# Performance work log

Hardware: AMD Instinct MI355X
Metric: run time of the kernel (lower is better)

The kernel has to match this reference:

```python
import jax, jax.numpy as jnp
import numpy as np

N, E = 10000, 160000
HID, EDIM = 256, 128
EPS = 1e-5


def _layernorm(x, g, b):
    mu = jnp.mean(x, axis=-1, keepdims=True)
    var = jnp.mean(jnp.square(x - mu), axis=-1, keepdims=True)
    return (x - mu) * jax.lax.rsqrt(var + EPS) * g + b


def setup_inputs() -> dict:
    key = jax.random.key(0)
    ks = jax.random.split(key, 12)
    cat_dim = 2 * HID + EDIM  # 640

    def lin(k, fan_in, fan_out):
        kw, kb = jax.random.split(k)
        lim = 1.0 / np.sqrt(fan_in)
        W = jax.random.uniform(kw, (fan_in, fan_out), jnp.float32, -lim, lim)
        b = jax.random.uniform(kb, (fan_out,), jnp.float32, -lim, lim)
        return W, b

    We1, be1 = lin(ks[0], cat_dim, EDIM)
    We2, be2 = lin(ks[1], EDIM, EDIM)
    Wv1, bv1 = lin(ks[2], cat_dim, HID)
    Wv2, bv2 = lin(ks[3], HID, HID)

    return {
        "h": jax.random.normal(ks[4], (N, HID), jnp.float32),
        "e": jax.random.normal(ks[5], (E, EDIM), jnp.float32),
        "edge_index": jax.random.randint(ks[6], (2, E), 0, N, jnp.int64),
        "We1": We1, "be1": be1, "We2": We2, "be2": be2,
        "Wv1": Wv1, "bv1": bv1, "Wv2": Wv2, "bv2": bv2,
        "ne_g": jnp.ones((EDIM,), jnp.float32), "ne_b": jnp.zeros((EDIM,), jnp.float32),
        "nv_g": jnp.ones((HID,), jnp.float32), "nv_b": jnp.zeros((HID,), jnp.float32),
    }


def reference(h, e, edge_index, We1, be1, We2, be2, Wv1, bv1, Wv2, bv2,
              ne_g, ne_b, nv_g, nv_b):
    # Eval mode: dropout and edge_drop are identity.
    src, dst = edge_index[0], edge_index[1]
    h_src = h[src]  # [E, HID] gather
    h_dst = h[dst]  # [E, HID] gather

    # Edge update: phi_e(concat) -> residual + LayerNorm
    xe = jnp.concatenate([h_src, h_dst, e], axis=-1)  # [E, 2H+ED]
    e_msg = jax.nn.gelu(xe @ We1 + be1, approximate=False) @ We2 + be2
    e_new = _layernorm(e + e_msg, ne_g, ne_b)

    # Node update: phi_v(concat with updated e) -> scatter_mean -> residual + LN
    xv = jnp.concatenate([h_src, h_dst, e_new], axis=-1)
    m = jax.nn.gelu(xv @ Wv1 + bv1, approximate=False) @ Wv2 + bv2  # [E, HID]
    agg = jax.ops.segment_sum(m, dst, num_segments=h.shape[0])
    counts = jax.ops.segment_sum(jnp.ones((m.shape[0], 1), m.dtype), dst,
                                 num_segments=h.shape[0])
    agg = agg / jnp.maximum(counts, 1.0)
    h_new = _layernorm(h + agg, nv_g, nv_b)
    return (h_new, e_new)
```

## Files before the change

kernel.cpp:

```cpp
#include <hip/hip_runtime.h>
#include <hip/hip_bf16.h>

#define NNODE 10000
#define NEDGE 160000
#define HIDD  256
#define ED    128
#define CAT   640

typedef short bf8 __attribute__((ext_vector_type(8)));
typedef short bf4 __attribute__((ext_vector_type(4)));
typedef float f4  __attribute__((ext_vector_type(4)));
typedef unsigned int u32;

__device__ __forceinline__ float bf2f(ushort u) {
    return __uint_as_float(((unsigned)u) << 16);
}
__device__ __forceinline__ ushort f2bf(float f) {
    unsigned u = __float_as_uint(f);
    return (ushort)((u + 0x7fffu + ((u >> 16) & 1u)) >> 16);
}
__device__ __forceinline__ float gelu_fast(float x) {
    float x2 = x * x;
    float u = 0.7978845608028654f * x * (1.0f + 0.044715f * x2);
    float au = fabsf(u);
    float ex = __expf(2.0f * au);
    float t = 1.0f - 2.0f / (1.0f + ex);
    t = copysignf(t, u);
    return 0.5f * x * (1.0f + t);
}
__device__ __forceinline__ int clampi(int v) {
    return ((unsigned)v >= (unsigned)NNODE) ? 0 : v;
}
__device__ __forceinline__ int getidx(const int* ei, bool i64, int pos) {
    int v = i64 ? ei[2 * pos] : ei[pos];
    return clampi(v);
}
__device__ __forceinline__ float loadf(const void* p, size_t idx, bool f32) {
    return f32 ? ((const float*)p)[idx] : bf2f(((const ushort*)p)[idx]);
}
__device__ __forceinline__ bf8 load8(const void* p, size_t idx, bool f32) {
    if (f32) {
        const float* fp = (const float*)p + idx;
        f4 lo = *(const f4*)fp, hi = *(const f4*)(fp + 4);
        bf8 r;
        r[0] = (short)f2bf(lo[0]); r[1] = (short)f2bf(lo[1]);
        r[2] = (short)f2bf(lo[2]); r[3] = (short)f2bf(lo[3]);
        r[4] = (short)f2bf(hi[0]); r[5] = (short)f2bf(hi[1]);
        r[6] = (short)f2bf(hi[2]); r[7] = (short)f2bf(hi[3]);
        return r;
    }
    return *(const bf8*)((const ushort*)p + idx);
}
__device__ __forceinline__ void storef(void* p, size_t idx, float v, bool f32) {
    if (f32) ((float*)p)[idx] = v;
    else     ((ushort*)p)[idx] = f2bf(v);
}
__device__ __forceinline__ void fadd_native(float* p, float v) {
    unsafeAtomicAdd(p, v);
}
__device__ __forceinline__ void detect_local(const u32* h_u32, const u32* ei_u32,
                                             u32* sf) {
    if (threadIdx.x < 64) {
        int t = threadIdx.x;
        u32 e8 = (h_u32[t] >> 7) & 0xFFu;
        bool inw = (e8 >= 100u && e8 <= 150u);
        unsigned long long m = __ballot(inw);
        bool hi_nz = (t < 16) ? (ei_u32[2 * t + 1] != 0u) : false;
        unsigned long long m2 = __ballot(hi_nz);
        if (t == 0) {
            sf[0] = (__popcll(m) < 40) ? 1u : 0u;
            sf[1] = (m2 == 0ull) ? 1u : 0u;
        }
    }
    __syncthreads();
}

#define PREP_B 1280
#define HCONV_B 1250
#define COUNT_B 625
__global__ __launch_bounds__(256) void combo_kernel(
    const void* __restrict__ h, const int* __restrict__ ei,
    const void* __restrict__ We1, const void* __restrict__ We2,
    const void* __restrict__ Wv1, const void* __restrict__ Wv2,
    ushort* __restrict__ WT, ushort* __restrict__ hb,
    u32* __restrict__ cnt, u32* __restrict__ flags)
{
    __shared__ u32 sf[2];
    detect_local((const u32*)h, (const u32*)ei, sf);
    const bool f32 = sf[0] != 0, i64 = sf[1] != 0;
    int b = blockIdx.x, tid = threadIdx.x;

    if (b == 0 && tid == 0) { flags[0] = sf[0]; flags[1] = sf[1]; }

    if (b < PREP_B) {
        int idx = b * 256 + tid;
        if (idx >= 327680) return;
        const void* W; int base, k0, K, Wld;
        if      (idx <  32768) { W = We1; base = 0;      k0 = 0;   K = 256; Wld = 128; }
        else if (idx <  65536) { W = We1; base = 32768;  k0 = 256; K = 256; Wld = 128; }
        else if (idx <  81920) { W = We1; base = 65536;  k0 = 512; K = 128; Wld = 128; }
        else if (idx <  98304) { W = We2; base = 81920;  k0 = 0;   K = 128; Wld = 128; }
        else if (idx < 163840) { W = Wv1; base = 98304;  k0 = 0;   K = 256; Wld = 256; }
        else if (idx < 229376) { W = Wv1; base = 163840; k0 = 256; K = 256; Wld = 256; }
        else if (idx < 262144) { W = Wv1; base = 229376; k0 = 512; K = 128; Wld = 256; }
        else                   { W = Wv2; base = 262144; k0 = 0;   K = 256; Wld = 256; }
        int local = idx - base;
        int k = local & (K - 1);
        int n = local / K;
        WT[idx] = f2bf(loadf(W, (size_t)(k0 + k) * Wld + n, f32));
    } else if (b < PREP_B + HCONV_B) {
        int i = (b - PREP_B) * 256 + tid;
        if (i < NNODE * HIDD / 8)
            *(bf8*)&hb[(size_t)i * 8] = load8(h, (size_t)i * 8, f32);
    } else {
        int i = (b - PREP_B - HCONV_B) * 256 + tid;
        if (i < NEDGE) atomicAdd(&cnt[getidx(ei, i64, NEDGE + i)], 1u);
    }
}

__global__ void scan_kernel(const u32* __restrict__ cnt, int* __restrict__ head) {
    __shared__ u32 part[256];
    __shared__ u32 base[256];
    int t = threadIdx.x;
    u32 s = 0;
    for (int j = 0; j < 40; ++j) {
        int i = t * 40 + j;
        if (i < NNODE) s += cnt[i];
    }
    part[t] = s;
    __syncthreads();
    if (t == 0) {
        u32 run = 0;
        for (int i = 0; i < 256; ++i) { base[i] = run; run += part[i]; }
    }
    __syncthreads();
    u32 run = base[t];
    for (int j = 0; j < 40; ++j) {
        int i = t * 40 + j;
        if (i < NNODE) { head[i] = (int)run; run += cnt[i]; }
    }
}

template<int NB>
__device__ __forceinline__ void qp_body(const ushort* __restrict__ hb,
                                        const ushort* __restrict__ WT,
                                        const void* __restrict__ bias,
                                        ushort* __restrict__ O, int bid, bool f32) {
    const int tid = threadIdx.x;
    const int wid = tid >> 6, lane = tid & 63;
    const int l16 = lane & 15, lg = lane >> 4;
    const int node0 = bid * 64;
    const int N = NB * 64;
    const int n0 = wid * (NB * 16);

    size_t ra[4];
    #pragma unroll
    for (int ai = 0; ai < 4; ++ai) {
        int row = node0 + ai * 16 + l16;
        ra[ai] = (size_t)(row < NNODE ? row : NNODE - 1) * HIDD;
    }
    int bb[NB];
    #pragma unroll
    for (int bi = 0; bi < NB; ++bi) bb[bi] = (n0 + bi * 16 + l16) * HIDD;

    f4 acc[4][NB] = {};
    for (int kc = 0; kc < 4; ++kc) {
        #pragma unroll
        for (int ks = 0; ks < 2; ++ks) {
            int kk = kc * 64 + ks * 32 + lg * 8;
            bf8 b[NB];
            #pragma unroll
            for (int bi = 0; bi < NB; ++bi) b[bi] = *(const bf8*)&WT[bb[bi] + kk];
            #pragma unroll
            for (int ai = 0; ai < 4; ++ai) {
                bf8 a = *(const bf8*)&hb[ra[ai] + kk];
                #pragma unroll
                for (int bi = 0; bi < NB; ++bi)
                    acc[ai][bi] = __builtin_amdgcn_mfma_f32_16x16x32_bf16(a, b[bi], acc[ai][bi], 0, 0, 0);
            }
        }
    }
    #pragma unroll
    for (int bi = 0; bi < NB; ++bi) {
        int col = n0 + bi * 16 + l16;
        int pcol; float badd;
        if constexpr (NB == 4) {
            int hh = col >> 7, c = col & 127;
            badd = (hh == 0) ? loadf(bias, c, f32) : 0.f;
            pcol = hh * 128 + (c & 15) * 8 + (c >> 4);
        } else {
            int hh = col >> 8, c = col & 255;
            badd = (hh == 0) ? loadf(bias, c, f32) : 0.f;
            int nh2 = c >> 7, rem = c & 127, w = rem >> 5, b2 = (rem >> 4) & 1, l = c & 15;
            pcol = hh * 256 + w * 64 + l * 4 + nh2 * 2 + b2;
        }
        #pragma unroll
        for (int ai = 0; ai < 4; ++ai)
            #pragma unroll
            for (int r = 0; r < 4; ++r) {
                int gr = node0 + ai * 16 + lg * 4 + r;
                if (gr < NNODE) O[(size_t)gr * N + pcol] = f2bf(acc[ai][bi][r] + badd);
            }
    }
}

#define QPB ((NNODE + 63) / 64)
#define FILL_B 625
__global__ __launch_bounds__(256) void fillqp_kernel(
    const int* __restrict__ ei, int* __restrict__ head,
    int* __restrict__ perm, int* __restrict__ dsts,
    const ushort* __restrict__ hb, const ushort* __restrict__ WTe,
    const ushort* __restrict__ WTv, const void* __restrict__ be1,
    const void* __restrict__ bv1, ushort* __restrict__ Qab,
    ushort* __restrict__ Pab, const u32* __restrict__ flags)
{
    const bool f32 = flags[0] != 0, i64 = flags[1] != 0;
    int b = blockIdx.x;
    if (b < FILL_B) {
        int i = b * 256 + threadIdx.x;
        if (i < NEDGE) {
            int d = getidx(ei, i64, NEDGE + i);
            int pos = atomicAdd(&head[d], 1);
            perm[pos] = i;
            dsts[pos] = d;
        }
    } else if (b < FILL_B + QPB) {
        qp_body<4>(hb, WTe, be1, Qab, b - FILL_B, f32);
    } else {
        qp_body<8>(hb, WTv, bv1, Pab, b - FILL_B - QPB, f32);
    }
}

#define FWG (NEDGE / 64)
__global__ __launch_bounds__(256) void fused_kernel(
    const void* __restrict__ e, const int* __restrict__ ei,
    const int* __restrict__ perm, const int* __restrict__ dsts,
    const ushort* __restrict__ WT1c,
    const ushort* __restrict__ WT2, const void* __restrict__ be2,
    const ushort* __restrict__ Qab,
    const void* __restrict__ neg, const void* __restrict__ neb,
    const ushort* __restrict__ WvcT,
    const ushort* __restrict__ Pab,
    float* __restrict__ S, void* __restrict__ out,
    const u32* __restrict__ flags)
{
    const bool f32 = flags[0] != 0, i64 = flags[1] != 0;
    __shared__ ushort Asm[64 * 136];
    __shared__ ushort Bsm[128 * 136];
    __shared__ ushort Tsm[64 * 136];
    __shared__ int PermS[64], SrcS[64], DstS[64];

    int orig = blockIdx.x;
    int xcd = orig & 7, slot = orig >> 3;
    int bid = (xcd < 4 ? xcd * 313 : 4 * 313 + (xcd - 4) * 312) + slot;

    const int tid = threadIdx.x;
    const int wid = tid >> 6, lane = tid & 63;
    const int l16 = lane & 15, lg = lane >> 4;
    const int edge0 = bid * 64;
    const int rm = wid * 16;

    if (tid < 64) {
        int eid = perm[edge0 + tid];
        PermS[tid] = eid;
        SrcS[tid] = getidx(ei, i64, eid);
        DstS[tid] = dsts[edge0 + tid];
    }
    __syncthreads();

    #pragma unroll
    for (int j = 0; j < 4; ++j) {
        int s2 = tid + j * 256;
        int r = s2 >> 4, c8 = (s2 & 15) * 8;
        *(bf8*)&Asm[r * 136 + c8] = load8(e, (size_t)PermS[r] * ED + c8, f32);
    }
    #pragma unroll
    for (int it = 0; it < 8; ++it) {
        int s2 = tid + it * 256;
        int n = s2 >> 4, c8 = (s2 & 15) * 8;
        *(bf8*)&Bsm[n * 136 + c8] = *(const bf8*)&WT1c[n * 128 + c8];
    }
    __syncthreads();

    f4 acc[8] = {};
    #pragma unroll
    for (int kc = 0; kc < 2; ++kc)
        #pragma unroll
        for (int ks = 0; ks < 2; ++ks) {
            int ko = kc * 64 + ks * 32 + lg * 8;
            bf8 a = *(const bf8*)&Asm[(rm + l16) * 136 + ko];
            #pragma unroll
            for (int f = 0; f < 8; ++f) {
                bf8 b = *(const bf8*)&Bsm[(f * 16 + l16) * 136 + ko];
                acc[f] = __builtin_amdgcn_mfma_f32_16x16x32_bf16(a, b, acc[f], 0, 0, 0);
            }
        }

    {
        bf8 qs[4], qd[4];
        #pragma unroll
        for (int r = 0; r < 4; ++r) {
            int row = rm + lg * 4 + r;
            qs[r] = *(const bf8*)&Qab[(size_t)SrcS[row] * 256 + l16 * 8];
            qd[r] = *(const bf8*)&Qab[(size_t)DstS[row] * 256 + 128 + l16 * 8];
        }
        #pragma unroll
        for (int f = 0; f < 8; ++f)
            #pragma unroll
            for (int r = 0; r < 4; ++r) {
                float val = acc[f][r] + bf2f((ushort)qs[r][f]) + bf2f((ushort)qd[r][f]);
                Tsm[(rm + lg * 4 + r) * 136 + f * 16 + l16] = f2bf(gelu_fast(val));
            }
    }
    __syncthreads();

    #pragma unroll
    for (int it = 0; it < 8; ++it) {
        int s2 = tid + it * 256;
        int n = s2 >> 4, c8 = (s2 & 15) * 8;
        *(bf8*)&Bsm[n * 136 + c8] = *(const bf8*)&WT2[n * 128 + c8];
    }
    __syncthreads();

    f4 acc2[8] = {};
    #pragma unroll
    for (int kc = 0; kc < 2; ++kc)
        #pragma unroll
        for (int ks = 0; ks < 2; ++ks) {
            int ko = kc * 64 + ks * 32 + lg * 8;
            bf8 a = *(const bf8*)&Tsm[(rm + l16) * 136 + ko];
            #pragma unroll
            for (int f = 0; f < 8; ++f) {
                bf8 b = *(const bf8*)&Bsm[(f * 16 + l16) * 136 + ko];
                acc2[f] = __builtin_amdgcn_mfma_f32_16x16x32_bf16(a, b, acc2[f], 0, 0, 0);
            }
        }

    {
        float v[8][4];
        #pragma unroll
        for (int f = 0; f < 8; ++f) {
            int col = f * 16 + l16;
            float bias = loadf(be2, col, f32);
            #pragma unroll
            for (int r = 0; r < 4; ++r) {
                int row = rm + lg * 4 + r;
                v[f][r] = acc2[f][r] + bias + bf2f(Asm[row * 136 + col]);
            }
        }
        #pragma unroll
        for (int r = 0; r < 4; ++r) {
            float s = 0.f;
            #pragma unroll
            for (int f = 0; f < 8; ++f) s += v[f][r];
            s += __shfl_xor(s, 1); s += __shfl_xor(s, 2);
            s += __shfl_xor(s, 4); s += __shfl_xor(s, 8);
            float mu = s * (1.0f / 128.0f);
            float q = 0.f;
            #pragma unroll
            for (int f = 0; f < 8; ++f) { float d = v[f][r] - mu; q += d * d; }
            q += __shfl_xor(q, 1); q += __shfl_xor(q, 2);
            q += __shfl_xor(q, 4); q += __shfl_xor(q, 8);
            float rstd = rsqrtf(q * (1.0f / 128.0f) + 1e-5f);
            int row = rm + lg * 4 + r;
            #pragma unroll
            for (int f = 0; f < 8; ++f) {
                int col = f * 16 + l16;
                float y = (v[f][r] - mu) * rstd * loadf(neg, col, f32) + loadf(neb, col, f32);
                Tsm[row * 136 + col] = f2bf(y);
            }
        }
    }
    __syncthreads();

    bf4 ps[4][4], pd[4][4];
    #pragma unroll
    for (int ai = 0; ai < 4; ++ai) {
        int p0 = ai * 16 + lg * 4;
        #pragma unroll
        for (int r = 0; r < 4; ++r) {
            ps[ai][r] = *(const bf4*)&Pab[(size_t)SrcS[p0 + r] * 512 + wid * 64 + l16 * 4];
            pd[ai][r] = *(const bf4*)&Pab[(size_t)DstS[p0 + r] * 512 + 256 + wid * 64 + l16 * 4];
        }
    }

    {
        int row = tid >> 2, pc = (tid & 3) * 32;
        size_t obase = (size_t)NNODE * HIDD + (size_t)PermS[row] * ED + pc;
        #pragma unroll
        for (int q2 = 0; q2 < 4; ++q2) {
            bf8 w = *(const bf8*)&Tsm[row * 136 + pc + q2 * 8];
            if (f32) {
                f4 lo, hi;
                lo[0] = bf2f((ushort)w[0]); lo[1] = bf2f((ushort)w[1]);
                lo[2] = bf2f((ushort)w[2]); lo[3] = bf2f((ushort)w[3]);
                hi[0] = bf2f((ushort)w[4]); hi[1] = bf2f((ushort)w[5]);
                hi[2] = bf2f((ushort)w[6]); hi[3] = bf2f((ushort)w[7]);
                *(f4*)((float*)out + obase + q2 * 8) = lo;
                *(f4*)((float*)out + obase + q2 * 8 + 4) = hi;
            } else {
                *(bf8*)((ushort*)out + obase + q2 * 8) = w;
            }
        }
    }

    f4 accN[4][2][2] = {};
    #pragma unroll
    for (int nh = 0; nh < 2; ++nh) {
        #pragma unroll
        for (int it = 0; it < 8; ++it) {
            int s2 = tid + it * 256;
            int n = s2 >> 4, c8 = (s2 & 15) * 8;
            *(bf8*)&Bsm[n * 136 + c8] = *(const bf8*)&WvcT[(nh * 128 + n) * 128 + c8];
        }
        __syncthreads();
        #pragma unroll
        for (int kc = 0; kc < 2; ++kc)
            #pragma unroll
            for (int ks = 0; ks < 2; ++ks) {
                int ko = kc * 64 + ks * 32 + lg * 8;
                bf8 a[4], b[2];
                #pragma unroll
                for (int ai = 0; ai < 4; ++ai)
                    a[ai] = *(const bf8*)&Tsm[(ai * 16 + l16) * 136 + ko];
                #pragma unroll
                for (int bi = 0; bi < 2; ++bi)
                    b[bi] = *(const bf8*)&Bsm[(wid * 32 + bi * 16 + l16) * 136 + ko];
                #pragma unroll
                for (int ai = 0; ai < 4; ++ai)
                    #pragma unroll
                    for (int bi = 0; bi < 2; ++bi)
                        accN[ai][nh][bi] = __builtin_amdgcn_mfma_f32_16x16x32_bf16(a[ai], b[bi], accN[ai][nh][bi], 0, 0, 0);
            }
        __syncthreads();
    }

    #pragma unroll
    for (int ai = 0; ai < 4; ++ai) {
        int p0 = ai * 16 + lg * 4;
        int dd[4];
        #pragma unroll
        for (int r = 0; r < 4; ++r) dd[r] = DstS[p0 + r];
        #pragma unroll
        for (int nh = 0; nh < 2; ++nh)
            #pragma unroll
            for (int bi = 0; bi < 2; ++bi) {
                int col = nh * 128 + wid * 32 + bi * 16 + l16;
                const int j = nh * 2 + bi;
                float v0 = gelu_fast(accN[ai][nh][bi][0] + bf2f((ushort)ps[ai][0][j]) + bf2f((ushort)pd[ai][0][j]));
                float v1 = gelu_fast(accN[ai][nh][bi][1] + bf2f((ushort)ps[ai][1][j]) + bf2f((ushort)pd[ai][1][j]));
                float v2 = gelu_fast(accN[ai][nh][bi][2] + bf2f((ushort)ps[ai][2][j]) + bf2f((ushort)pd[ai][2][j]));
                float v3 = gelu_fast(accN[ai][nh][bi][3] + bf2f((ushort)ps[ai][3][j]) + bf2f((ushort)pd[ai][3][j]));
                float s = v0; int d = dd[0];
                if (dd[1] == d) s += v1; else { fadd_native(&S[(size_t)d * HIDD + col], s); d = dd[1]; s = v1; }
                if (dd[2] == d) s += v2; else { fadd_native(&S[(size_t)d * HIDD + col], s); d = dd[2]; s = v2; }
                if (dd[3] == d) s += v3; else { fadd_native(&S[(size_t)d * HIDD + col], s); d = dd[3]; s = v3; }
                fadd_native(&S[(size_t)d * HIDD + col], s);
            }
    }
}

__global__ __launch_bounds__(256) void hn_gemm_kernel(
    const float* __restrict__ S, const ushort* __restrict__ WTv2,
    const void* __restrict__ bv2, const u32* __restrict__ cnt,
    const void* __restrict__ h,
    const void* __restrict__ nvg, const void* __restrict__ nvb,
    void* __restrict__ out, const u32* __restrict__ flags)
{
    const bool f32 = flags[0] != 0;
    constexpr int LDV = 260;
    __shared__ float Vsm[64 * LDV];

    const int tid = threadIdx.x;
    const int wid = tid >> 6, lane = tid & 63;
    const int l16 = lane & 15, lg = lane >> 4;
    const int node0 = blockIdx.x * 64;
    const int n0 = wid * 64;

    size_t ra[4];
    #pragma unroll
    for (int ai = 0; ai < 4; ++ai) {
        int row = node0 + ai * 16 + l16;
        ra[ai] = (size_t)(row < NNODE ? row : NNODE - 1) * HIDD;
    }
    int bb[4];
    #pragma unroll
    for (int bi = 0; bi < 4; ++bi) bb[bi] = (n0 + bi * 16 + l16) * HIDD;

    f4 acc[4][4] = {};
    for (int kc = 0; kc < 4; ++kc) {
        #pragma unroll
        for (int ks = 0; ks < 2; ++ks) {
            int kk = kc * 64 + ks * 32 + lg * 8;
            bf8 b[4];
            #pragma unroll
            for (int bi = 0; bi < 4; ++bi) b[bi] = *(const bf8*)&WTv2[bb[bi] + kk];
            #pragma unroll
            for (int ai = 0; ai < 4; ++ai) {
                bf8 a = load8(S, ra[ai] + kk, true);
                #pragma unroll
                for (int bi = 0; bi < 4; ++bi)
                    acc[ai][bi] = __builtin_amdgcn_mfma_f32_16x16x32_bf16(a, b[bi], acc[ai][bi], 0, 0, 0);
            }
        }
    }

    #pragma unroll
    for (int bi = 0; bi < 4; ++bi) {
        int col = n0 + bi * 16 + l16;
        float b2 = loadf(bv2, col, f32);
        #pragma unroll
        for (int ai = 0; ai < 4; ++ai)
            #pragma unroll
            for (int r = 0; r < 4; ++r) {
                int rowl = ai * 16 + lg * 4 + r;
                int gr = node0 + rowl;
                int grc = gr < NNODE ? gr : NNODE - 1;
                float c = (float)cnt[grc];
                float inv = 1.0f / fmaxf(c, 1.0f);
                float val = (acc[ai][bi][r] + c * b2) * inv
                          + loadf(h, (size_t)grc * HIDD + col, f32);
                Vsm[rowl * LDV + col] = val;
            }
    }
    __syncthreads();

    #pragma unroll
    for (int rr = 0; rr < 4; ++rr) {
        int rowl = wid * 16 + lg * 4 + rr;
        int gr = node0 + rowl;
        float x[16];
        #pragma unroll
        for (int f = 0; f < 16; ++f) x[f] = Vsm[rowl * LDV + f * 16 + l16];
        float s = 0.f;
        #pragma unroll
        for (int f = 0; f < 16; ++f) s += x[f];
        s += __shfl_xor(s, 1); s += __shfl_xor(s, 2);
        s += __shfl_xor(s, 4); s += __shfl_xor(s, 8);
        float mu = s * (1.0f / 256.0f);
        float q = 0.f;
        #pragma unroll
        for (int f = 0; f < 16; ++f) { float d = x[f] - mu; q += d * d; }
        q += __shfl_xor(q, 1); q += __shfl_xor(q, 2);
        q += __shfl_xor(q, 4); q += __shfl_xor(q, 8);
        float rstd = rsqrtf(q * (1.0f / 256.0f) + 1e-5f);
        if (gr < NNODE) {
            #pragma unroll
            for (int f = 0; f < 16; ++f) {
                int col = f * 16 + l16;
                float y = (x[f] - mu) * rstd * loadf(nvg, col, f32) + loadf(nvb, col, f32);
                storef(out, (size_t)gr * HIDD + col, y, f32);
            }
        }
    }
}

extern "C" void kernel_launch(void* const* d_in, const int* in_sizes, int n_in,
                              void* d_out, int out_size, void* d_ws, size_t ws_size,
                              hipStream_t stream)
{
    (void)in_sizes; (void)n_in; (void)out_size; (void)ws_size;
    const void* h   = d_in[0];
    const void* e   = d_in[1];
    const int*  ei  = (const int*)d_in[2];
    const void* We1 = d_in[3];
    const void* be1 = d_in[4];
    const void* We2 = d_in[5];
    const void* be2 = d_in[6];
    const void* Wv1 = d_in[7];
    const void* bv1 = d_in[8];
    const void* Wv2 = d_in[9];
    const void* bv2 = d_in[10];
    const void* neg = d_in[11];
    const void* neb = d_in[12];
    const void* nvg = d_in[13];
    const void* nvb = d_in[14];

    char* ws = (char*)d_ws;
    u32*   flags = (u32*)ws;
    float* S     = (float*)(ws + 256);
    u32*   cnt   = (u32*)(ws + 256 + (size_t)NNODE * HIDD * 4);
    size_t off = 256 + (size_t)NNODE * HIDD * 4 + ((size_t)NNODE * 4 + 255) / 256 * 256;
    int*   head = (int*)(ws + off);            off += ((size_t)NNODE * 4 + 255) / 256 * 256;
    int*   perm = (int*)(ws + off);            off += (size_t)NEDGE * 4;
    int*   dsts = (int*)(ws + off);            off += (size_t)NEDGE * 4;
    ushort* WTb  = (ushort*)(ws + off);
    ushort* WTe  = WTb;
    ushort* WT1c = WTb + 65536;
    ushort* WT2  = WTb + 81920;
    ushort* WTv  = WTb + 98304;
    ushort* WvcT = WTb + 229376;
    ushort* WTv2 = WTb + 262144;
    ushort* hb   = WTb + 327680;
    ushort* Qab  = hb + (size_t)NNODE * HIDD;
    ushort* Pab  = Qab + (size_t)NNODE * 256;

    hipMemsetAsync(S, 0, (size_t)NNODE * HIDD * 4 + (size_t)NNODE * 4, stream);

    combo_kernel<<<PREP_B + HCONV_B + COUNT_B, 256, 0, stream>>>(
        h, ei, We1, We2, Wv1, Wv2, WTb, hb, cnt, flags);
    scan_kernel<<<1, 256, 0, stream>>>(cnt, head);
    fillqp_kernel<<<FILL_B + 2 * QPB, 256, 0, stream>>>(
        ei, head, perm, dsts, hb, WTe, WTv, be1, bv1, Qab, Pab, flags);

    fused_kernel<<<FWG, 256, 0, stream>>>(e, ei, perm, dsts,
                                          WT1c, WT2, be2, Qab,
                                          neg, neb, WvcT, Pab,
                                          S, d_out, flags);
    hn_gemm_kernel<<<(NNODE + 63) / 64, 256, 0, stream>>>(S, WTv2, bv2, cnt, h,
                                                          nvg, nvb, d_out, flags);
}
```

Baseline: 330.2 us.

## Drop h bf16 staging, zero S in combo kernel, read Wvc directly

The separate bf16 copy of h is removed; the Q/P projection GEMMs now convert h on the fly from the original input. The large memset of the scatter accumulator S moves into extra blocks of the combo kernel, leaving only a small memset for the counts. In the fused kernel the Wvc weight tile is no longer staged through shared memory with two barriers per half; each wave loads its B fragments straight from global memory. This trades less staging traffic and fewer syncs for repeated global and L2 weight reads and conversion work inside the GEMM loop.

```diff
diff --git a/kernel.cpp b/kernel.cpp
--- a/kernel.cpp
+++ b/kernel.cpp
@@ -76,13 +76,13 @@
 }
 
 #define PREP_B 1280
-#define HCONV_B 1250
 #define COUNT_B 625
+#define SZERO_B 2500
 __global__ __launch_bounds__(256) void combo_kernel(
     const void* __restrict__ h, const int* __restrict__ ei,
     const void* __restrict__ We1, const void* __restrict__ We2,
     const void* __restrict__ Wv1, const void* __restrict__ Wv2,
-    ushort* __restrict__ WT, ushort* __restrict__ hb,
+    ushort* __restrict__ WT, float* __restrict__ S,
     u32* __restrict__ cnt, u32* __restrict__ flags)
 {
     __shared__ u32 sf[2];
@@ -108,13 +108,15 @@
         int k = local & (K - 1);
         int n = local / K;
         WT[idx] = f2bf(loadf(W, (size_t)(k0 + k) * Wld + n, f32));
-    } else if (b < PREP_B + HCONV_B) {
+    } else if (b < PREP_B + COUNT_B) {
         int i = (b - PREP_B) * 256 + tid;
-        if (i < NNODE * HIDD / 8)
-            *(bf8*)&hb[(size_t)i * 8] = load8(h, (size_t)i * 8, f32);
+        if (i < NEDGE) atomicAdd(&cnt[getidx(ei, i64, NEDGE + i)], 1u);
     } else {
-        int i = (b - PREP_B - HCONV_B) * 256 + tid;
-        if (i < NEDGE) atomicAdd(&cnt[getidx(ei, i64, NEDGE + i)], 1u);
+        size_t i = (size_t)(b - PREP_B - COUNT_B) * 256 + tid;
+        if (i < (size_t)NNODE * HIDD / 4) {
+            f4 z = {};
+            *(f4*)&S[i * 4] = z;
+        }
     }
 }
 
@@ -142,7 +144,7 @@
 }
 
 template<int NB>
-__device__ __forceinline__ void qp_body(const ushort* __restrict__ hb,
+__device__ __forceinline__ void qp_body(const void* __restrict__ h,
                                         const ushort* __restrict__ WT,
                                         const void* __restrict__ bias,
                                         ushort* __restrict__ O, int bid, bool f32) {
@@ -173,7 +175,7 @@
             for (int bi = 0; bi < NB; ++bi) b[bi] = *(const bf8*)&WT[bb[bi] + kk];
             #pragma unroll
             for (int ai = 0; ai < 4; ++ai) {
-                bf8 a = *(const bf8*)&hb[ra[ai] + kk];
+                bf8 a = load8(h, ra[ai] + kk, f32);
                 #pragma unroll
                 for (int bi = 0; bi < NB; ++bi)
                     acc[ai][bi] = __builtin_amdgcn_mfma_f32_16x16x32_bf16(a, b[bi], acc[ai][bi], 0, 0, 0);
@@ -209,7 +211,7 @@
 __global__ __launch_bounds__(256) void fillqp_kernel(
     const int* __restrict__ ei, int* __restrict__ head,
     int* __restrict__ perm, int* __restrict__ dsts,
-    const ushort* __restrict__ hb, const ushort* __restrict__ WTe,
+    const void* __restrict__ h, const ushort* __restrict__ WTe,
     const ushort* __restrict__ WTv, const void* __restrict__ be1,
     const void* __restrict__ bv1, ushort* __restrict__ Qab,
     ushort* __restrict__ Pab, const u32* __restrict__ flags)
@@ -225,9 +227,9 @@
             dsts[pos] = d;
         }
     } else if (b < FILL_B + QPB) {
-        qp_body<4>(hb, WTe, be1, Qab, b - FILL_B, f32);
+        qp_body<4>(h, WTe, be1, Qab, b - FILL_B, f32);
     } else {
-        qp_body<8>(hb, WTv, bv1, Pab, b - FILL_B - QPB, f32);
+        qp_body<8>(h, WTv, bv1, Pab, b - FILL_B - QPB, f32);
     }
 }
 
@@ -406,14 +408,7 @@
 
     f4 accN[4][2][2] = {};
     #pragma unroll
-    for (int nh = 0; nh < 2; ++nh) {
-        #pragma unroll
-        for (int it = 0; it < 8; ++it) {
-            int s2 = tid + it * 256;
-            int n = s2 >> 4, c8 = (s2 & 15) * 8;
-            *(bf8*)&Bsm[n * 136 + c8] = *(const bf8*)&WvcT[(nh * 128 + n) * 128 + c8];
-        }
-        __syncthreads();
+    for (int nh = 0; nh < 2; ++nh)
         #pragma unroll
         for (int kc = 0; kc < 2; ++kc)
             #pragma unroll
@@ -421,19 +416,17 @@
                 int ko = kc * 64 + ks * 32 + lg * 8;
                 bf8 a[4], b[2];
                 #pragma unroll
+                for (int bi = 0; bi < 2; ++bi)
+                    b[bi] = *(const bf8*)&WvcT[(nh * 128 + wid * 32 + bi * 16 + l16) * 128 + ko];
+                #pragma unroll
                 for (int ai = 0; ai < 4; ++ai)
                     a[ai] = *(const bf8*)&Tsm[(ai * 16 + l16) * 136 + ko];
-                #pragma unroll
-                for (int bi = 0; bi < 2; ++bi)
-                    b[bi] = *(const bf8*)&Bsm[(wid * 32 + bi * 16 + l16) * 136 + ko];
                 #pragma unroll
                 for (int ai = 0; ai < 4; ++ai)
                     #pragma unroll
                     for (int bi = 0; bi < 2; ++bi)
                         accN[ai][nh][bi] = __builtin_amdgcn_mfma_f32_16x16x32_bf16(a[ai], b[bi], accN[ai][nh][bi], 0, 0, 0);
             }
-        __syncthreads();
-    }
 
     #pragma unroll
     for (int ai = 0; ai < 4; ++ai) {
@@ -591,17 +584,16 @@
     ushort* WTv  = WTb + 98304;
     ushort* WvcT = WTb + 229376;
     ushort* WTv2 = WTb + 262144;
-    ushort* hb   = WTb + 327680;
-    ushort* Qab  = hb + (size_t)NNODE * HIDD;
+    ushort* Qab  = WTb + 327680;
     ushort* Pab  = Qab + (size_t)NNODE * 256;
 
-    hipMemsetAsync(S, 0, (size_t)NNODE * HIDD * 4 + (size_t)NNODE * 4, stream);
-
-    combo_kernel<<<PREP_B + HCONV_B + COUNT_B, 256, 0, stream>>>(
-        h, ei, We1, We2, Wv1, Wv2, WTb, hb, cnt, flags);
+    hipMemsetAsync(cnt, 0, (size_t)NNODE * 4, stream);
+
+    combo_kernel<<<PREP_B + COUNT_B + SZERO_B, 256, 0, stream>>>(
+        h, ei, We1, We2, Wv1, Wv2, WTb, S, cnt, flags);
     scan_kernel<<<1, 256, 0, stream>>>(cnt, head);
     fillqp_kernel<<<FILL_B + 2 * QPB, 256, 0, stream>>>(
-        ei, head, perm, dsts, hb, WTe, WTv, be1, bv1, Qab, Pab, flags);
+        ei, head, perm, dsts, h, WTe, WTv, be1, bv1, Qab, Pab, flags);
 
     fused_kernel<<<FWG, 256, 0, stream>>>(e, ei, perm, dsts,
                                           WT1c, WT2, be2, Qab,
```

Measured after the change: 339.7 us. 2.9% more time.

## Load weight tiles directly into LDS with XOR-swizzled layout

Applied to the files above, without the earlier changes.

Weight tiles for the three in-kernel GEMMs now go straight from global memory into shared memory through the global_load_lds builtin, bypassing registers. The padded 136-stride layout is replaced by a dense 128-stride layout. To avoid bank conflicts, the prep kernel pre-swizzles the K index of the affected weight blocks with an XOR pattern, and the MFMA B-operand reads apply the matching XOR. This trims register pressure and VGPR round-trips on the weight staging, but correctness depends on every WT1c/WT2/WvcT source being stored swizzled to match.

```diff
diff --git a/kernel.cpp b/kernel.cpp
--- a/kernel.cpp
+++ b/kernel.cpp
@@ -57,6 +57,11 @@
 }
 __device__ __forceinline__ void fadd_native(float* p, float v) {
     unsafeAtomicAdd(p, v);
+}
+__device__ __forceinline__ void gload16(const void* g, void* l) {
+    __builtin_amdgcn_global_load_lds(
+        (const __attribute__((address_space(1))) void*)g,
+        (__attribute__((address_space(3))) void*)l, 16, 0, 0);
 }
 __device__ __forceinline__ void detect_local(const u32* h_u32, const u32* ei_u32,
                                              u32* sf) {
@@ -95,19 +100,20 @@
     if (b < PREP_B) {
         int idx = b * 256 + tid;
         if (idx >= 327680) return;
-        const void* W; int base, k0, K, Wld;
+        const void* W; int base, k0, K, Wld; bool swz = false;
         if      (idx <  32768) { W = We1; base = 0;      k0 = 0;   K = 256; Wld = 128; }
         else if (idx <  65536) { W = We1; base = 32768;  k0 = 256; K = 256; Wld = 128; }
-        else if (idx <  81920) { W = We1; base = 65536;  k0 = 512; K = 128; Wld = 128; }
-        else if (idx <  98304) { W = We2; base = 81920;  k0 = 0;   K = 128; Wld = 128; }
+        else if (idx <  81920) { W = We1; base = 65536;  k0 = 512; K = 128; Wld = 128; swz = true; }
+        else if (idx <  98304) { W = We2; base = 81920;  k0 = 0;   K = 128; Wld = 128; swz = true; }
         else if (idx < 163840) { W = Wv1; base = 98304;  k0 = 0;   K = 256; Wld = 256; }
         else if (idx < 229376) { W = Wv1; base = 163840; k0 = 256; K = 256; Wld = 256; }
-        else if (idx < 262144) { W = Wv1; base = 229376; k0 = 512; K = 128; Wld = 256; }
+        else if (idx < 262144) { W = Wv1; base = 229376; k0 = 512; K = 128; Wld = 256; swz = true; }
         else                   { W = Wv2; base = 262144; k0 = 0;   K = 256; Wld = 256; }
         int local = idx - base;
         int k = local & (K - 1);
         int n = local / K;
-        WT[idx] = f2bf(loadf(W, (size_t)(k0 + k) * Wld + n, f32));
+        int kd = swz ? (k ^ ((n & 7) << 3)) : k;
+        WT[base + n * K + kd] = f2bf(loadf(W, (size_t)(k0 + k) * Wld + n, f32));
     } else if (b < PREP_B + HCONV_B) {
         int i = (b - PREP_B) * 256 + tid;
         if (i < NNODE * HIDD / 8)
@@ -246,7 +252,7 @@
 {
     const bool f32 = flags[0] != 0, i64 = flags[1] != 0;
     __shared__ ushort Asm[64 * 136];
-    __shared__ ushort Bsm[128 * 136];
+    __shared__ ushort Bsm[128 * 128];
     __shared__ ushort Tsm[64 * 136];
     __shared__ int PermS[64], SrcS[64], DstS[64];
 
@@ -259,6 +265,7 @@
     const int l16 = lane & 15, lg = lane >> 4;
     const int edge0 = bid * 64;
     const int rm = wid * 16;
+    const int sx = (l16 & 7) << 3;
 
     if (tid < 64) {
         int eid = perm[edge0 + tid];
@@ -269,17 +276,17 @@
     __syncthreads();
 
     #pragma unroll
+    for (int it = 0; it < 8; ++it) {
+        int r0 = it * 16 + wid * 4;
+        gload16(WT1c + (size_t)(r0 + (lane >> 4)) * 128 + (lane & 15) * 8,
+                &Bsm[r0 * 128]);
+    }
+    #pragma unroll
     for (int j = 0; j < 4; ++j) {
         int s2 = tid + j * 256;
         int r = s2 >> 4, c8 = (s2 & 15) * 8;
         *(bf8*)&Asm[r * 136 + c8] = load8(e, (size_t)PermS[r] * ED + c8, f32);
     }
-    #pragma unroll
-    for (int it = 0; it < 8; ++it) {
-        int s2 = tid + it * 256;
-        int n = s2 >> 4, c8 = (s2 & 15) * 8;
-        *(bf8*)&Bsm[n * 136 + c8] = *(const bf8*)&WT1c[n * 128 + c8];
-    }
     __syncthreads();
 
     f4 acc[8] = {};
@@ -288,10 +295,11 @@
         #pragma unroll
         for (int ks = 0; ks < 2; ++ks) {
             int ko = kc * 64 + ks * 32 + lg * 8;
+            int kos = ko ^ sx;
             bf8 a = *(const bf8*)&Asm[(rm + l16) * 136 + ko];
             #pragma unroll
             for (int f = 0; f < 8; ++f) {
-                bf8 b = *(const bf8*)&Bsm[(f * 16 + l16) * 136 + ko];
+                bf8 b = *(const bf8*)&Bsm[(f * 16 + l16) * 128 + kos];
                 acc[f] = __builtin_amdgcn_mfma_f32_16x16x32_bf16(a, b, acc[f], 0, 0, 0);
             }
         }
@@ -316,9 +324,9 @@
 
     #pragma unroll
     for (int it = 0; it < 8; ++it) {
-        int s2 = tid + it * 256;
-        int n = s2 >> 4, c8 = (s2 & 15) * 8;
-        *(bf8*)&Bsm[n * 136 + c8] = *(const bf8*)&WT2[n * 128 + c8];
+        int r0 = it * 16 + wid * 4;
+        gload16(WT2 + (size_t)(r0 + (lane >> 4)) * 128 + (lane & 15) * 8,
+                &Bsm[r0 * 128]);
     }
     __syncthreads();
 
@@ -328,10 +336,11 @@
         #pragma unroll
         for (int ks = 0; ks < 2; ++ks) {
             int ko = kc * 64 + ks * 32 + lg * 8;
+            int kos = ko ^ sx;
             bf8 a = *(const bf8*)&Tsm[(rm + l16) * 136 + ko];
             #pragma unroll
             for (int f = 0; f < 8; ++f) {
-                bf8 b = *(const bf8*)&Bsm[(f * 16 + l16) * 136 + ko];
+                bf8 b = *(const bf8*)&Bsm[(f * 16 + l16) * 128 + kos];
                 acc2[f] = __builtin_amdgcn_mfma_f32_16x16x32_bf16(a, b, acc2[f], 0, 0, 0);
             }
         }
@@ -409,9 +418,9 @@
     for (int nh = 0; nh < 2; ++nh) {
         #pragma unroll
         for (int it = 0; it < 8; ++it) {
-            int s2 = tid + it * 256;
-            int n = s2 >> 4, c8 = (s2 & 15) * 8;
-            *(bf8*)&Bsm[n * 136 + c8] = *(const bf8*)&WvcT[(nh * 128 + n) * 128 + c8];
+            int r0 = it * 16 + wid * 4;
+            gload16(WvcT + (size_t)(nh * 128 + r0 + (lane >> 4)) * 128 + (lane & 15) * 8,
+                    &Bsm[r0 * 128]);
         }
         __syncthreads();
         #pragma unroll
@@ -419,13 +428,14 @@
             #pragma unroll
             for (int ks = 0; ks < 2; ++ks) {
                 int ko = kc * 64 + ks * 32 + lg * 8;
+                int kos = ko ^ sx;
                 bf8 a[4], b[2];
                 #pragma unroll
                 for (int ai = 0; ai < 4; ++ai)
                     a[ai] = *(const bf8*)&Tsm[(ai * 16 + l16) * 136 + ko];
                 #pragma unroll
                 for (int bi = 0; bi < 2; ++bi)
-                    b[bi] = *(const bf8*)&Bsm[(wid * 32 + bi * 16 + l16) * 136 + ko];
+                    b[bi] = *(const bf8*)&Bsm[(wid * 32 + bi * 16 + l16) * 128 + kos];
                 #pragma unroll
                 for (int ai = 0; ai < 4; ++ai)
                     #pragma unroll
```

Result: no change. 326.6 us (-1.1%).
